# Performance work log

Hardware: AMD Instinct MI355X
Metric: run time of the kernel (lower is better)

Reference implementation:

```python
import jax, jax.numpy as jnp
import numpy as np

N = 100000   # num nodes
E = 3200000  # num edges (avg degree 32)
H = 64       # hidden_dim
EPS = 1e-5   # batchnorm eps


def setup_inputs() -> dict:
    key = jax.random.key(0)
    ks = jax.random.split(key, 12)
    def gl(k, shp):  # glorot-ish init
        fan = shp[0]
        return jax.random.normal(k, shp, dtype=jnp.float32) / np.sqrt(fan)
    return dict(
        x=jax.random.normal(ks[0], (N, 4), dtype=jnp.float32),
        src=jax.random.randint(ks[1], (E,), 0, N, dtype=jnp.int32),
        dst=jax.random.randint(ks[2], (E,), 0, N, dtype=jnp.int32),
        W0=gl(ks[3], (4, H)), b0=jnp.zeros((H,), jnp.float32),
        W1=gl(ks[4], (H, H)), b1=jnp.zeros((H,), jnp.float32),
        g0=jnp.ones((H,), jnp.float32), be0=jnp.zeros((H,), jnp.float32),
        g1=jnp.ones((H,), jnp.float32), be1=jnp.zeros((H,), jnp.float32),
        Wm0=gl(ks[5], (H, H)), bm0=jnp.zeros((H,), jnp.float32),
        Wm1=gl(ks[6], (H, H // 2)), bm1=jnp.zeros((H // 2,), jnp.float32),
        Wm2=gl(ks[7], (H // 2, 1)), bm2=jnp.zeros((1,), jnp.float32),
    )


def gcn_conv(x, W, b, src, dst, n):
    # PyG GCNConv: add self-loops, symmetric D^-1/2 (A+I) D^-1/2 normalization,
    # linear transform, scatter-add aggregation at destination, then bias.
    h = x @ W                                   # [n, out]
    loop = jnp.arange(n, dtype=src.dtype)
    s = jnp.concatenate([src, loop])            # sources incl self-loops
    d = jnp.concatenate([dst, loop])            # targets incl self-loops
    deg = jax.ops.segment_sum(jnp.ones_like(d, dtype=h.dtype), d, num_segments=n)
    dinv = jnp.where(deg > 0, jax.lax.rsqrt(deg), 0.0)
    norm = dinv[s] * dinv[d]                    # [E+n]
    msg = h[s] * norm[:, None]                  # gather + scale
    out = jax.ops.segment_sum(msg, d, num_segments=n)  # scatter-add
    return out + b


def batchnorm(x, g, b):
    # training-mode BatchNorm1d over the node dimension (biased variance)
    mu = jnp.mean(x, axis=0)
    var = jnp.mean(jnp.square(x - mu), axis=0)
    return g * (x - mu) * jax.lax.rsqrt(var + EPS) + b


def reference(x, src, dst, W0, b0, W1, b1, g0, be0, g1, be1,
              Wm0, bm0, Wm1, bm1, Wm2, bm2):
    n = x.shape[0]
    h = gcn_conv(x, W0, b0, src, dst, n)
    h = jax.nn.relu(batchnorm(h, g0, be0))      # dropout = identity (eval)
    h = gcn_conv(h, W1, b1, src, dst, n)
    h = jax.nn.relu(batchnorm(h, g1, be1))
    h = jax.nn.relu(h @ Wm0 + bm0)
    h = jax.nn.relu(h @ Wm1 + bm1)
    return jax.nn.sigmoid(h @ Wm2 + bm2)        # [n, 1] collision probs
```

## Files before the change

### kernel.cpp

```cpp
#include <hip/hip_runtime.h>
#include <hip/hip_fp16.h>
#include <math.h>

#define HD 64
#define EPS 1e-5f
#define BSH 9
#define BSZ 512
#define T1 16384

__device__ __forceinline__ float atomAddF(float* p, float v) {
    return unsafeAtomicAdd(p, v);
}


__global__ __launch_bounds__(256) void k_bhist(const int* __restrict__ dst,
        int* __restrict__ bcnt, int e) {
    __shared__ int h[256];
    int t = threadIdx.x;
    h[t] = 0;
    __syncthreads();
    for (int i = blockIdx.x * 256 + t; i < e; i += gridDim.x * 256)
        atomicAdd(&h[dst[i] >> BSH], 1);
    __syncthreads();
    if (h[t]) atomicAdd(&bcnt[t], h[t]);
}

__global__ __launch_bounds__(256) void k_bscan(const int* __restrict__ bcnt,
        int* __restrict__ boff, int* __restrict__ gcur,
        int* __restrict__ row_ptr, int nb, int n, int e) {
    __shared__ int sc[256];
    int t = threadIdx.x;
    int v = (t < nb) ? bcnt[t] : 0;
    sc[t] = v;
    __syncthreads();
    int acc = v;
    for (int off = 1; off < 256; off <<= 1) {
        int x = (t >= off) ? sc[t - off] : 0;
        __syncthreads();
        acc += x;
        sc[t] = acc;
        __syncthreads();
    }
    int ex = acc - v;
    boff[t] = ex;
    gcur[t] = ex;
    if (t == 0) row_ptr[n] = e;
}

__global__ __launch_bounds__(256) void k_bucket(const int* __restrict__ src,
        const int* __restrict__ dst, int* __restrict__ gcur,
        unsigned* __restrict__ bedges, int e) {
    __shared__ int hist[256];
    __shared__ int base[256];
    int t = threadIdx.x;
    for (int tile = blockIdx.x * T1; tile < e; tile += gridDim.x * T1) {
        int lim = min(e - tile, T1);
        hist[t] = 0;
        __syncthreads();
        for (int j = t; j < lim; j += 256)
            atomicAdd(&hist[dst[tile + j] >> BSH], 1);
        __syncthreads();
        int h = hist[t];
        int mybase = (h > 0) ? atomicAdd(&gcur[t], h) : 0;
        __syncthreads();
        hist[t] = 0;
        base[t] = mybase;
        __syncthreads();
        for (int j = t; j < lim; j += 256) {
            int d = dst[tile + j], s = src[tile + j];
            int bk = d >> BSH;
            int loc = atomicAdd(&hist[bk], 1);
            bedges[base[bk] + loc] = ((unsigned)(d & (BSZ - 1)) << 17) | (unsigned)s;
        }
        __syncthreads();
    }
}

__global__ __launch_bounds__(256) void k_build(const unsigned* __restrict__ bedges,
        const int* __restrict__ boff, int* __restrict__ row_ptr,
        unsigned* __restrict__ csr, float* __restrict__ dinv, int n) {
    __shared__ int hist[BSZ];
    __shared__ int cur[BSZ];
    __shared__ int sc[256];
    int b = blockIdx.x, t = threadIdx.x;
    int nodebase = b << BSH;
    int beg = boff[b], end = boff[b + 1];
    hist[t] = 0; hist[t + 256] = 0;
    __syncthreads();
    for (int j = beg + t; j < end; j += 256)
        atomicAdd(&hist[bedges[j] >> 17], 1);
    __syncthreads();
    int a0 = hist[2 * t], a1 = hist[2 * t + 1];
    int psum = a0 + a1;
    sc[t] = psum;
    __syncthreads();
    int acc = psum;
    for (int off = 1; off < 256; off <<= 1) {
        int x = (t >= off) ? sc[t - off] : 0;
        __syncthreads();
        acc += x;
        sc[t] = acc;
        __syncthreads();
    }
    int excl = acc - psum;
    int e0 = beg + excl, e1 = beg + excl + a0;
    cur[2 * t] = e0;
    cur[2 * t + 1] = e1;
    int n0 = nodebase + 2 * t, n1 = nodebase + 2 * t + 1;
    if (n0 < n) { row_ptr[n0] = e0; dinv[n0] = rsqrtf((float)(a0 + 1)); }
    if (n1 < n) { row_ptr[n1] = e1; dinv[n1] = rsqrtf((float)(a1 + 1)); }
    __syncthreads();
    for (int j = beg + t; j < end; j += 256) {
        unsigned p = bedges[j];
        int pos = atomicAdd(&cur[p >> 17], 1);
        csr[pos] = p;
    }
}


__global__ __launch_bounds__(256) void k_lin0(const float* __restrict__ x,
        const float* __restrict__ W0, const float* __restrict__ dinv,
        __half* __restrict__ A, int n_nodes) {
    __shared__ float w[4 * HD];
    int t = threadIdx.x;
    w[t] = W0[t];
    __syncthreads();
    int n = blockIdx.x * 4 + (t >> 6);
    int c = t & 63;
    if (n >= n_nodes) return;
    float x0 = x[n * 4 + 0], x1 = x[n * 4 + 1], x2 = x[n * 4 + 2], x3 = x[n * 4 + 3];
    float v = x0 * w[c] + x1 * w[64 + c] + x2 * w[128 + c] + x3 * w[192 + c];
    A[((size_t)n << 6) + c] = __float2half(v * dinv[n]);
}

__global__ __launch_bounds__(256) void k_aggr(const int* __restrict__ row_ptr,
        const unsigned* __restrict__ pedges, const __half* __restrict__ A,
        const float* __restrict__ dinv, const float* __restrict__ bias,
        float* __restrict__ B, float* __restrict__ stats, int n_nodes) {
    __shared__ float acc[64 * 65];
    __shared__ float ls[4][64], ls2[4][64];
    int t = threadIdx.x;
    for (int i = t; i < 64 * 65; i += 256) acc[i] = 0.f;
    int nodebase = blockIdx.x << 6;
    int nend = min(nodebase + 64, n_nodes);
    int ebeg = row_ptr[nodebase];
    int eend = row_ptr[nend];
    int nedges = eend - ebeg;
    __syncthreads();

    int wv = t >> 6, lane = t & 63;
    int sub = lane >> 4, ch = lane & 15;
    int s = wv * 4 + sub;
    int sbeg = ebeg + (int)(((long long)nedges * s) >> 4);
    int send = ebeg + (int)(((long long)nedges * (s + 1)) >> 4);
    const uint2* A2 = (const uint2*)A;

    float a0 = 0.f, a1 = 0.f, a2 = 0.f, a3 = 0.f;
    int cur = -1;

    #define FLUSH() if (cur >= 0) {                                            \
        int o_ = cur * 65 + (ch << 2);                                         \
        atomicAdd(&acc[o_ + 0], a0); atomicAdd(&acc[o_ + 1], a1);              \
        atomicAdd(&acc[o_ + 2], a2); atomicAdd(&acc[o_ + 3], a3); }

    #define PROC(P, U) {                                                       \
        int d_ = (int)((P) >> 17) & 63;                                        \
        if (d_ != cur) { FLUSH(); a0 = a1 = a2 = a3 = 0.f; cur = d_; }         \
        float2 f01_ = __half22float2(*(const __half2*)&(U).x);                 \
        float2 f23_ = __half22float2(*(const __half2*)&(U).y);                 \
        a0 += f01_.x; a1 += f01_.y; a2 += f23_.x; a3 += f23_.y; }

    int j = sbeg;
    for (; j + 8 <= send; j += 8) {
        unsigned p[8];
        uint2 u[8];
        #pragma unroll
        for (int k = 0; k < 8; ++k) p[k] = pedges[j + k];
        #pragma unroll
        for (int k = 0; k < 8; ++k)
            u[k] = A2[(((size_t)(p[k] & 0x1FFFFu)) << 4) + ch];
        #pragma unroll
        for (int k = 0; k < 8; ++k) PROC(p[k], u[k]);
    }
    for (; j < send; ++j) {
        unsigned p0 = pedges[j];
        uint2 u0 = A2[(((size_t)(p0 & 0x1FFFFu)) << 4) + ch];
        PROC(p0, u0);
    }
    FLUSH();
    #undef PROC
    #undef FLUSH
    __syncthreads();

    int c = lane;
    float st = 0.f, st2 = 0.f;
    for (int r = wv; r < 64; r += 4) {
        int node = nodebase + r;
        if (node < n_nodes) {
            float v = acc[r * 65 + c] + __half2float(A[((size_t)node << 6) + c]);
            v = dinv[node] * v + bias[c];
            B[((size_t)node << 6) + c] = v;
            st += v; st2 += v * v;
        }
    }
    ls[wv][c] = st; ls2[wv][c] = st2;
    __syncthreads();
    if (t < 64) {
        atomAddF(&stats[t], ls[0][t] + ls[1][t] + ls[2][t] + ls[3][t]);
        atomAddF(&stats[64 + t], ls2[0][t] + ls2[1][t] + ls2[2][t] + ls2[3][t]);
    }
}

__global__ __launch_bounds__(256) void k_lin1(const float* __restrict__ B,
        const float* __restrict__ W, const float* __restrict__ dinv,
        const float* __restrict__ stats, const float* __restrict__ g,
        const float* __restrict__ be, __half* __restrict__ A, int n_nodes) {
    __shared__ float w[HD * HD];
    __shared__ float rows[4][HD];
    int t = threadIdx.x;
    for (int i = t; i < HD * HD; i += 256) w[i] = W[i];
    int wv = t >> 6, c = t & 63;
    float inv_n = 1.0f / (float)n_nodes;
    float mu = stats[c] * inv_n;
    float var = stats[64 + c] * inv_n - mu * mu;
    float sc = g[c] * rsqrtf(var + EPS);
    float sh = be[c] - mu * sc;
    int ngroups = (n_nodes + 3) >> 2;
    for (int gidx = blockIdx.x; gidx < ngroups; gidx += gridDim.x) {
        __syncthreads();
        int n = gidx * 4 + wv;
        float rv = (n < n_nodes) ? fmaxf(sc * B[((size_t)n << 6) + c] + sh, 0.f) : 0.f;
        rows[wv][c] = rv;
        __syncthreads();
        if (n < n_nodes) {
            float acc = 0.f;
            #pragma unroll
            for (int k = 0; k < HD; k++) acc = fmaf(rows[wv][k], w[k * 64 + c], acc);
            A[((size_t)n << 6) + c] = __float2half(acc * dinv[n]);
        }
    }
}

__global__ __launch_bounds__(64) void k_mlp(const float* __restrict__ B,
        const float* __restrict__ stats, const float* __restrict__ g,
        const float* __restrict__ be,
        const float* __restrict__ Wm0, const float* __restrict__ bm0,
        const float* __restrict__ Wm1, const float* __restrict__ bm1,
        const float* __restrict__ Wm2, const float* __restrict__ bm2,
        float* __restrict__ out, int n_nodes) {
    __shared__ float rows[64][65];
    int t = threadIdx.x;
    float inv_n = 1.0f / (float)n_nodes;
    float mu = stats[t] * inv_n;
    float var = stats[64 + t] * inv_n - mu * mu;
    float sc = g[t] * rsqrtf(var + EPS);
    float sh = be[t] - mu * sc;
    int nbase = blockIdx.x * 64;
    #pragma unroll 4
    for (int r = 0; r < 64; r++) {
        int nn = nbase + r;
        rows[r][t] = (nn < n_nodes) ? fmaxf(sc * B[((size_t)nn << 6) + t] + sh, 0.f) : 0.f;
    }
    __syncthreads();
    int n = nbase + t;
    if (n >= n_nodes) return;

    float a1[64];
    #pragma unroll
    for (int cc = 0; cc < 4; ++cc) {
        float acc[16];
        #pragma unroll
        for (int j = 0; j < 16; ++j) acc[j] = bm0[cc * 16 + j];
        for (int k = 0; k < 64; ++k) {
            float hv = rows[t][k];
            #pragma unroll
            for (int j = 0; j < 16; ++j)
                acc[j] = fmaf(hv, Wm0[k * 64 + cc * 16 + j], acc[j]);
        }
        #pragma unroll
        for (int j = 0; j < 16; ++j) a1[cc * 16 + j] = fmaxf(acc[j], 0.f);
    }
    #pragma unroll
    for (int k = 0; k < 64; ++k) rows[t][k] = a1[k];

    float a2[32];
    #pragma unroll
    for (int cc = 0; cc < 2; ++cc) {
        float acc[16];
        #pragma unroll
        for (int j = 0; j < 16; ++j) acc[j] = bm1[cc * 16 + j];
        for (int k = 0; k < 64; ++k) {
            float hv = rows[t][k];
            #pragma unroll
            for (int j = 0; j < 16; ++j)
                acc[j] = fmaf(hv, Wm1[k * 32 + cc * 16 + j], acc[j]);
        }
        #pragma unroll
        for (int j = 0; j < 16; ++j) a2[cc * 16 + j] = fmaxf(acc[j], 0.f);
    }
    float z = bm2[0];
    #pragma unroll
    for (int k = 0; k < 32; ++k) z = fmaf(a2[k], Wm2[k], z);
    out[n] = 1.0f / (1.0f + __expf(-z));
}

extern "C" void kernel_launch(void* const* d_in, const int* in_sizes, int n_in,
                              void* d_out, int out_size, void* d_ws, size_t ws_size,
                              hipStream_t stream) {
    const float* x   = (const float*)d_in[0];
    const int*   src = (const int*)d_in[1];
    const int*   dst = (const int*)d_in[2];
    const float* W0  = (const float*)d_in[3];
    const float* b0  = (const float*)d_in[4];
    const float* W1  = (const float*)d_in[5];
    const float* b1  = (const float*)d_in[6];
    const float* g0  = (const float*)d_in[7];
    const float* be0 = (const float*)d_in[8];
    const float* g1  = (const float*)d_in[9];
    const float* be1 = (const float*)d_in[10];
    const float* Wm0 = (const float*)d_in[11];
    const float* bm0 = (const float*)d_in[12];
    const float* Wm1 = (const float*)d_in[13];
    const float* bm1 = (const float*)d_in[14];
    const float* Wm2 = (const float*)d_in[15];
    const float* bm2 = (const float*)d_in[16];

    int n = in_sizes[0] / 4;
    int e = in_sizes[1];
    float* out = (float*)d_out;

    char* ws = (char*)d_ws;
    auto alignup = [](size_t v) { return (v + 255) & ~(size_t)255; };
    size_t o = 0;
    int*      bcnt    = (int*)(ws + o);      o += alignup(256 * 4);
    int*      boff    = (int*)(ws + o);      o += alignup(257 * 4);
    int*      gcur    = (int*)(ws + o);      o += alignup(256 * 4);
    float*    stats   = (float*)(ws + o);    o += alignup(256 * 4);
    int*      row_ptr = (int*)(ws + o);      o += alignup((size_t)(n + 1) * 4);
    float*    dinv    = (float*)(ws + o);    o += alignup((size_t)n * 4);
    unsigned* bedges  = (unsigned*)(ws + o); o += alignup((size_t)e * 4);
    unsigned* csr     = (unsigned*)(ws + o); o += alignup((size_t)e * 4);
    __half*   A       = (__half*)(ws + o);   o += alignup((size_t)n * 64 * 2);
    float*    B       = (float*)(ws + o);

    int nb     = (n + BSZ - 1) >> BSH;
    int gN4    = (n + 3) / 4;
    int ntiles = (e + T1 - 1) / T1;
    int gMLP   = (n + 63) / 64;
    int gAGG   = (n + 63) / 64;

    (void)hipMemsetAsync(bcnt, 0, 256 * 4, stream);
    (void)hipMemsetAsync(stats, 0, 256 * 4, stream);

    k_bhist<<<512, 256, 0, stream>>>(dst, bcnt, e);
    k_bscan<<<1, 256, 0, stream>>>(bcnt, boff, gcur, row_ptr, nb, n, e);
    k_bucket<<<ntiles, 256, 0, stream>>>(src, dst, gcur, bedges, e);
    k_build<<<nb, 256, 0, stream>>>(bedges, boff, row_ptr, csr, dinv, n);

    k_lin0<<<gN4, 256, 0, stream>>>(x, W0, dinv, A, n);
    k_aggr<<<gAGG, 256, 0, stream>>>(row_ptr, csr, A, dinv, b0, B, stats, n);

    k_lin1<<<2048, 256, 0, stream>>>(B, W1, dinv, stats, g0, be0, A, n);
    k_aggr<<<gAGG, 256, 0, stream>>>(row_ptr, csr, A, dinv, b1, B, stats + 128, n);

    k_mlp<<<gMLP, 64, 0, stream>>>(B, stats + 128, g1, be1,
                                   Wm0, bm0, Wm1, bm1, Wm2, bm2, out, n);
}
```

Baseline: 401.1 us.

## Split feature table into channel planes and aggregate per plane for cache locality

Stores the fp16 node feature table as four 16-channel planes and launches the aggregation kernel once per plane, so each pass gathers from a smaller working set that is more likely to stay cache-resident. Each lane now handles 4 channels of one of 64 edge segments per block. The epilogue uses wave shuffles for the BN statistics reduction. Edge-list loads become nontemporal. The trade-off is reading the edge list and row pointers four times per layer and issuing more kernel launches.

```diff
diff --git a/kernel.cpp b/kernel.cpp
--- a/kernel.cpp
+++ b/kernel.cpp
@@ -130,17 +130,18 @@
     if (n >= n_nodes) return;
     float x0 = x[n * 4 + 0], x1 = x[n * 4 + 1], x2 = x[n * 4 + 2], x3 = x[n * 4 + 3];
     float v = x0 * w[c] + x1 * w[64 + c] + x2 * w[128 + c] + x3 * w[192 + c];
-    A[((size_t)n << 6) + c] = __float2half(v * dinv[n]);
+    size_t pbase = (size_t)(c >> 4) * ((size_t)n_nodes << 4);
+    A[pbase + ((size_t)n << 4) + (c & 15)] = __float2half(v * dinv[n]);
 }
 
 __global__ __launch_bounds__(256) void k_aggr(const int* __restrict__ row_ptr,
         const unsigned* __restrict__ pedges, const __half* __restrict__ A,
         const float* __restrict__ dinv, const float* __restrict__ bias,
-        float* __restrict__ B, float* __restrict__ stats, int n_nodes) {
-    __shared__ float acc[64 * 65];
-    __shared__ float ls[4][64], ls2[4][64];
-    int t = threadIdx.x;
-    for (int i = t; i < 64 * 65; i += 256) acc[i] = 0.f;
+        float* __restrict__ B, float* __restrict__ stats, int n_nodes, int plane) {
+    __shared__ float acc[64 * 17];
+    __shared__ float ls[4][16], ls2[4][16];
+    int t = threadIdx.x;
+    for (int i = t; i < 64 * 17; i += 256) acc[i] = 0.f;
     int nodebase = blockIdx.x << 6;
     int nend = min(nodebase + 64, n_nodes);
     int ebeg = row_ptr[nodebase];
@@ -149,17 +150,18 @@
     __syncthreads();
 
     int wv = t >> 6, lane = t & 63;
-    int sub = lane >> 4, ch = lane & 15;
-    int s = wv * 4 + sub;
-    int sbeg = ebeg + (int)(((long long)nedges * s) >> 4);
-    int send = ebeg + (int)(((long long)nedges * (s + 1)) >> 4);
-    const uint2* A2 = (const uint2*)A;
+    int sub = lane >> 2, ch = lane & 3;
+    int s = wv * 16 + sub;
+    int sbeg = ebeg + (int)(((long long)nedges * s) >> 6);
+    int send = ebeg + (int)(((long long)nedges * (s + 1)) >> 6);
+    const __half* Ap = A + (size_t)plane * ((size_t)n_nodes << 4);
+    const uint2* A2 = (const uint2*)Ap;
 
     float a0 = 0.f, a1 = 0.f, a2 = 0.f, a3 = 0.f;
     int cur = -1;
 
     #define FLUSH() if (cur >= 0) {                                            \
-        int o_ = cur * 65 + (ch << 2);                                         \
+        int o_ = cur * 17 + (ch << 2);                                         \
         atomicAdd(&acc[o_ + 0], a0); atomicAdd(&acc[o_ + 1], a1);              \
         atomicAdd(&acc[o_ + 2], a2); atomicAdd(&acc[o_ + 3], a3); }
 
@@ -175,16 +177,16 @@
         unsigned p[8];
         uint2 u[8];
         #pragma unroll
-        for (int k = 0; k < 8; ++k) p[k] = pedges[j + k];
+        for (int k = 0; k < 8; ++k) p[k] = __builtin_nontemporal_load(&pedges[j + k]);
         #pragma unroll
         for (int k = 0; k < 8; ++k)
-            u[k] = A2[(((size_t)(p[k] & 0x1FFFFu)) << 4) + ch];
+            u[k] = A2[(((size_t)(p[k] & 0x1FFFFu)) << 2) + ch];
         #pragma unroll
         for (int k = 0; k < 8; ++k) PROC(p[k], u[k]);
     }
     for (; j < send; ++j) {
-        unsigned p0 = pedges[j];
-        uint2 u0 = A2[(((size_t)(p0 & 0x1FFFFu)) << 4) + ch];
+        unsigned p0 = __builtin_nontemporal_load(&pedges[j]);
+        uint2 u0 = A2[(((size_t)(p0 & 0x1FFFFu)) << 2) + ch];
         PROC(p0, u0);
     }
     FLUSH();
@@ -192,22 +194,29 @@
     #undef FLUSH
     __syncthreads();
 
-    int c = lane;
+    int c = lane & 15;
+    int rbase = wv * 4 + (lane >> 4);
+    int cglob = (plane << 4) + c;
+    float bc = bias[cglob];
     float st = 0.f, st2 = 0.f;
-    for (int r = wv; r < 64; r += 4) {
+    for (int r = rbase; r < 64; r += 16) {
         int node = nodebase + r;
         if (node < n_nodes) {
-            float v = acc[r * 65 + c] + __half2float(A[((size_t)node << 6) + c]);
-            v = dinv[node] * v + bias[c];
-            B[((size_t)node << 6) + c] = v;
+            float v = acc[r * 17 + c] + __half2float(Ap[((size_t)node << 4) + c]);
+            v = dinv[node] * v + bc;
+            B[((size_t)node << 6) + cglob] = v;
             st += v; st2 += v * v;
         }
     }
-    ls[wv][c] = st; ls2[wv][c] = st2;
-    __syncthreads();
-    if (t < 64) {
-        atomAddF(&stats[t], ls[0][t] + ls[1][t] + ls[2][t] + ls[3][t]);
-        atomAddF(&stats[64 + t], ls2[0][t] + ls2[1][t] + ls2[2][t] + ls2[3][t]);
+    st += __shfl_xor(st, 16, 64);  st += __shfl_xor(st, 32, 64);
+    st2 += __shfl_xor(st2, 16, 64); st2 += __shfl_xor(st2, 32, 64);
+    if (lane < 16) { ls[wv][c] = st; ls2[wv][c] = st2; }
+    __syncthreads();
+    if (t < 16) {
+        atomAddF(&stats[cglob - c + t],
+                 ls[0][t] + ls[1][t] + ls[2][t] + ls[3][t]);
+        atomAddF(&stats[64 + cglob - c + t],
+                 ls2[0][t] + ls2[1][t] + ls2[2][t] + ls2[3][t]);
     }
 }
 
@@ -225,6 +234,8 @@
     float var = stats[64 + c] * inv_n - mu * mu;
     float sc = g[c] * rsqrtf(var + EPS);
     float sh = be[c] - mu * sc;
+    size_t pbase = (size_t)(c >> 4) * ((size_t)n_nodes << 4);
+    int cc = c & 15;
     int ngroups = (n_nodes + 3) >> 2;
     for (int gidx = blockIdx.x; gidx < ngroups; gidx += gridDim.x) {
         __syncthreads();
@@ -236,7 +247,7 @@
             float acc = 0.f;
             #pragma unroll
             for (int k = 0; k < HD; k++) acc = fmaf(rows[wv][k], w[k * 64 + c], acc);
-            A[((size_t)n << 6) + c] = __float2half(acc * dinv[n]);
+            A[pbase + ((size_t)n << 4) + cc] = __float2half(acc * dinv[n]);
         }
     }
 }
@@ -358,10 +369,12 @@
     k_build<<<nb, 256, 0, stream>>>(bedges, boff, row_ptr, csr, dinv, n);
 
     k_lin0<<<gN4, 256, 0, stream>>>(x, W0, dinv, A, n);
-    k_aggr<<<gAGG, 256, 0, stream>>>(row_ptr, csr, A, dinv, b0, B, stats, n);
+    for (int p = 0; p < 4; ++p)
+        k_aggr<<<gAGG, 256, 0, stream>>>(row_ptr, csr, A, dinv, b0, B, stats, n, p);
 
     k_lin1<<<2048, 256, 0, stream>>>(B, W1, dinv, stats, g0, be0, A, n);
-    k_aggr<<<gAGG, 256, 0, stream>>>(row_ptr, csr, A, dinv, b1, B, stats + 128, n);
+    for (int p = 0; p < 4; ++p)
+        k_aggr<<<gAGG, 256, 0, stream>>>(row_ptr, csr, A, dinv, b1, B, stats + 128, n, p);
 
     k_mlp<<<gMLP, 64, 0, stream>>>(B, stats + 128, g1, be1,
                                    Wm0, bm0, Wm1, bm1, Wm2, bm2, out, n);
```

Result: slower. 587.5 us (+46.5%).

## Restructure MLP head kernel to channel-parallel threads with shuffle reduction

Applied to the files above, without the earlier changes.

The MLP kernel moves from one thread per node to 256-thread blocks handling 32 nodes, with each thread owning an output channel across 8 rows. The first two layers read activations from shared memory as float2 with coalesced weight loads. The final 32-wide dot product is done with a warp shuffle reduction. This is meant to cut register pressure and raise occupancy and parallelism in the tail kernel, in exchange for extra block barriers and shuffles.

```diff
diff --git a/kernel.cpp b/kernel.cpp
--- a/kernel.cpp
+++ b/kernel.cpp
@@ -241,67 +241,91 @@
     }
 }
 
-__global__ __launch_bounds__(64) void k_mlp(const float* __restrict__ B,
+__global__ __launch_bounds__(256) void k_mlp(const float* __restrict__ B,
         const float* __restrict__ stats, const float* __restrict__ g,
         const float* __restrict__ be,
         const float* __restrict__ Wm0, const float* __restrict__ bm0,
         const float* __restrict__ Wm1, const float* __restrict__ bm1,
         const float* __restrict__ Wm2, const float* __restrict__ bm2,
         float* __restrict__ out, int n_nodes) {
-    __shared__ float rows[64][65];
-    int t = threadIdx.x;
-    float inv_n = 1.0f / (float)n_nodes;
-    float mu = stats[t] * inv_n;
-    float var = stats[64 + t] * inv_n - mu * mu;
-    float sc = g[t] * rsqrtf(var + EPS);
-    float sh = be[t] - mu * sc;
-    int nbase = blockIdx.x * 64;
+    __shared__ float rows[32][66];
+    __shared__ float scb[64], shb[64];
+    int t = threadIdx.x;
+    if (t < 64) {
+        float inv_n = 1.0f / (float)n_nodes;
+        float mu = stats[t] * inv_n;
+        float var = stats[64 + t] * inv_n - mu * mu;
+        float sc = g[t] * rsqrtf(var + EPS);
+        scb[t] = sc;
+        shb[t] = be[t] - mu * sc;
+    }
+    __syncthreads();
+    int nbase = blockIdx.x * 32;
+    #pragma unroll 8
+    for (int i = 0; i < 8; ++i) {
+        int idx = t + i * 256;
+        int r = idx >> 6, c = idx & 63;
+        int nn = nbase + r;
+        float v = (nn < n_nodes) ? B[((size_t)nn << 6) + c] : 0.f;
+        rows[r][c] = fmaxf(scb[c] * v + shb[c], 0.f);
+    }
+    __syncthreads();
+
+    int w = t >> 6, j = t & 63;
+    int rb = w * 8;
+    float acc0[8];
+    float b0j = bm0[j];
+    #pragma unroll
+    for (int i = 0; i < 8; ++i) acc0[i] = b0j;
     #pragma unroll 4
-    for (int r = 0; r < 64; r++) {
-        int nn = nbase + r;
-        rows[r][t] = (nn < n_nodes) ? fmaxf(sc * B[((size_t)nn << 6) + t] + sh, 0.f) : 0.f;
-    }
-    __syncthreads();
-    int n = nbase + t;
-    if (n >= n_nodes) return;
-
-    float a1[64];
-    #pragma unroll
-    for (int cc = 0; cc < 4; ++cc) {
-        float acc[16];
-        #pragma unroll
-        for (int j = 0; j < 16; ++j) acc[j] = bm0[cc * 16 + j];
-        for (int k = 0; k < 64; ++k) {
-            float hv = rows[t][k];
-            #pragma unroll
-            for (int j = 0; j < 16; ++j)
-                acc[j] = fmaf(hv, Wm0[k * 64 + cc * 16 + j], acc[j]);
-        }
-        #pragma unroll
-        for (int j = 0; j < 16; ++j) a1[cc * 16 + j] = fmaxf(acc[j], 0.f);
-    }
-    #pragma unroll
-    for (int k = 0; k < 64; ++k) rows[t][k] = a1[k];
-
-    float a2[32];
-    #pragma unroll
-    for (int cc = 0; cc < 2; ++cc) {
-        float acc[16];
-        #pragma unroll
-        for (int j = 0; j < 16; ++j) acc[j] = bm1[cc * 16 + j];
-        for (int k = 0; k < 64; ++k) {
-            float hv = rows[t][k];
-            #pragma unroll
-            for (int j = 0; j < 16; ++j)
-                acc[j] = fmaf(hv, Wm1[k * 32 + cc * 16 + j], acc[j]);
-        }
-        #pragma unroll
-        for (int j = 0; j < 16; ++j) a2[cc * 16 + j] = fmaxf(acc[j], 0.f);
-    }
-    float z = bm2[0];
-    #pragma unroll
-    for (int k = 0; k < 32; ++k) z = fmaf(a2[k], Wm2[k], z);
-    out[n] = 1.0f / (1.0f + __expf(-z));
+    for (int k = 0; k < 64; k += 2) {
+        float wv0 = Wm0[k * 64 + j];
+        float wv1 = Wm0[(k + 1) * 64 + j];
+        #pragma unroll
+        for (int i = 0; i < 8; ++i) {
+            float2 hv = *(const float2*)&rows[rb + i][k];
+            acc0[i] = fmaf(hv.x, wv0, acc0[i]);
+            acc0[i] = fmaf(hv.y, wv1, acc0[i]);
+        }
+    }
+    #pragma unroll
+    for (int i = 0; i < 8; ++i) rows[rb + i][j] = fmaxf(acc0[i], 0.f);
+    __syncthreads();
+    int h = j >> 5, ch2 = j & 31;
+    int rb1 = rb + h * 4;
+    float acc2[4];
+    float b1j = bm1[ch2];
+    #pragma unroll
+    for (int i = 0; i < 4; ++i) acc2[i] = b1j;
+    #pragma unroll 4
+    for (int k = 0; k < 64; k += 2) {
+        float wv0 = Wm1[k * 32 + ch2];
+        float wv1 = Wm1[(k + 1) * 32 + ch2];
+        #pragma unroll
+        for (int i = 0; i < 4; ++i) {
+            float2 hv = *(const float2*)&rows[rb1 + i][k];
+            acc2[i] = fmaf(hv.x, wv0, acc2[i]);
+            acc2[i] = fmaf(hv.y, wv1, acc2[i]);
+        }
+    }
+    float wm2 = Wm2[ch2];
+    float z[4];
+    #pragma unroll
+    for (int i = 0; i < 4; ++i) z[i] = fmaxf(acc2[i], 0.f) * wm2;
+    #pragma unroll
+    for (int d = 1; d < 32; d <<= 1) {
+        #pragma unroll
+        for (int i = 0; i < 4; ++i) z[i] += __shfl_xor(z[i], d, 64);
+    }
+    if (ch2 == 0) {
+        float bb = bm2[0];
+        #pragma unroll
+        for (int i = 0; i < 4; ++i) {
+            int nn = nbase + rb1 + i;
+            if (nn < n_nodes)
+                out[nn] = 1.0f / (1.0f + __expf(-(z[i] + bb)));
+        }
+    }
 }
 
 extern "C" void kernel_launch(void* const* d_in, const int* in_sizes, int n_in,
@@ -346,7 +370,7 @@
     int nb     = (n + BSZ - 1) >> BSH;
     int gN4    = (n + 3) / 4;
     int ntiles = (e + T1 - 1) / T1;
-    int gMLP   = (n + 63) / 64;
+    int gMLP   = (n + 31) / 32;
     int gAGG   = (n + 63) / 64;
 
     (void)hipMemsetAsync(bcnt, 0, 256 * 4, stream);
@@ -363,6 +387,6 @@
     k_lin1<<<2048, 256, 0, stream>>>(B, W1, dinv, stats, g0, be0, A, n);
     k_aggr<<<gAGG, 256, 0, stream>>>(row_ptr, csr, A, dinv, b1, B, stats + 128, n);
 
-    k_mlp<<<gMLP, 64, 0, stream>>>(B, stats + 128, g1, be1,
-                                   Wm0, bm0, Wm1, bm1, Wm2, bm2, out, n);
-}
+    k_mlp<<<gMLP, 256, 0, stream>>>(B, stats + 128, g1, be1,
+                                    Wm0, bm0, Wm1, bm1, Wm2, bm2, out, n);
+}
```

Result: no change. 395.6 us (-1.4%).
